# Kernel tuning notes

Hardware: AMD Instinct MI355X
Metric: run time of the kernel (lower is better)

## Reference

```python
import jax, jax.numpy as jnp
from jax import lax
import numpy as np

B, T, F = 256, 2048, 12
EV_VOCAB, RS_VOCAB = 32, 8
EED, RED = 6, 3
H, K = 96, 3
D = F + EED + RED  # 21


def setup_inputs() -> dict:
    key = jax.random.key(0)
    ks = jax.random.split(key, 12)
    s = 0.05
    return {
        'seq': jax.random.normal(ks[0], (B, T, F), jnp.float32),
        'ev': jax.random.randint(ks[1], (B, T), 0, EV_VOCAB),
        'rs': jax.random.randint(ks[2], (B, T), 0, RS_VOCAB),
        'lengths': jax.random.randint(ks[3], (B,), 1, T + 1),  # valid lengths in [1, T]
        'event_emb': jax.random.normal(ks[4], (EV_VOCAB, EED), jnp.float32) * s,
        'result_emb': jax.random.normal(ks[5], (RS_VOCAB, RED), jnp.float32) * s,
        'W_ih': jax.random.normal(ks[6], (4 * H, D), jnp.float32) * s,
        'W_hh': jax.random.normal(ks[7], (4 * H, H), jnp.float32) * s,
        'b_ih': jnp.zeros((4 * H,), jnp.float32),
        'b_hh': jnp.zeros((4 * H,), jnp.float32),
        'W_mlp': jax.random.normal(ks[8], (H, H * K), jnp.float32) * s,
        'b_mlp': jnp.zeros((H,), jnp.float32),
        'W_fc': jax.random.normal(ks[9], (2, 2 * H), jnp.float32) * s,
        'b_fc': jnp.zeros((2,), jnp.float32),
    }


def reference(seq, ev, rs, lengths, event_emb, result_emb, W_ih, W_hh, b_ih, b_hh,
              W_mlp, b_mlp, W_fc, b_fc):
    # embed + concat -> [B,T,D]
    x = jnp.concatenate([seq, event_emb[ev], result_emb[rs]], axis=-1)
    xs = jnp.swapaxes(x, 0, 1)  # [T,B,D]
    ts = jnp.arange(T)
    b = b_ih + b_hh

    def step(carry, inp):
        h, c = carry
        x_t, t = inp
        gates = x_t @ W_ih.T + h @ W_hh.T + b  # [B,4H]
        i, f, g, o = jnp.split(gates, 4, axis=-1)  # PyTorch gate order i,f,g,o
        i = jax.nn.sigmoid(i); f = jax.nn.sigmoid(f)
        g = jnp.tanh(g); o = jax.nn.sigmoid(o)
        c_new = f * c + i * g
        h_new = o * jnp.tanh(c_new)
        m = (t < lengths)[:, None]  # packed-seq semantics: freeze state past length
        h = jnp.where(m, h_new, h)
        c = jnp.where(m, c_new, c)
        out = jnp.where(m, h_new, jnp.zeros_like(h_new))  # pad_packed zeros
        return (h, c), out

    h0 = jnp.zeros((B, H), x.dtype)
    (h_fin, _), outs = lax.scan(step, (h0, h0), (xs, ts))
    out_padded = jnp.swapaxes(outs, 0, 1)  # [B,T,H]

    # vectorized last-k gather (replaces torch Python loop)
    idx = lengths[:, None] - K + jnp.arange(K)  # [B,K]
    valid = idx >= 0
    gathered = jnp.take_along_axis(out_padded, jnp.clip(idx, 0)[:, :, None], axis=1)
    gathered = jnp.where(valid[:, :, None], gathered, jnp.zeros_like(gathered))
    lastk = gathered.reshape(B, K * H)

    h_lastk = jax.nn.relu(lastk @ W_mlp.T + b_mlp)
    h = jnp.concatenate([h_fin, h_lastk], axis=1)  # [B,2H]
    return h @ W_fc.T + b_fc  # [B,2]
```

## Files before the change

### kernel.cpp

```cpp
#include <hip/hip_runtime.h>

#define TT 2048
#define FF 12
#define HH 96
#define NG 384
#define CK 64
#define NT 768
#define L2E 1.44269504088896340736f

typedef __attribute__((ext_vector_type(2))) float f2;
typedef __attribute__((ext_vector_type(4))) float f4;

__device__ __forceinline__ float fast_exp2(float x){ return __builtin_amdgcn_exp2f(x); }
__device__ __forceinline__ float fast_rcp(float x){ return __builtin_amdgcn_rcpf(x); }
__device__ __forceinline__ float sigm(float x){
  return fast_rcp(1.f + fast_exp2(-L2E * x));
}
__device__ __forceinline__ float tanh_f(float x){
  const float e = fast_exp2((-2.f*L2E)*fabsf(x));
  return copysignf((1.f - e) * fast_rcp(1.f + e), x);
}

__global__ __launch_bounds__(NT, 3) void lstm_persist(
  const float* __restrict__ seq, const int* __restrict__ ev, const int* __restrict__ rsi,
  const int* __restrict__ len, const float* __restrict__ eemb, const float* __restrict__ remb,
  const float* __restrict__ W_ih, const float* __restrict__ W_hh,
  const float* __restrict__ b_ih, const float* __restrict__ b_hh,
  const float* __restrict__ W_mlp, const float* __restrict__ b_mlp,
  const float* __restrict__ W_fc, const float* __restrict__ b_fc,
  float* __restrict__ out)
{
  const int b   = blockIdx.x;
  const int tid = threadIdx.x;
  const int w   = tid >> 6;
  const int l   = tid & 63;
  const int s   = w & 3;
  const int gg  = w >> 2;
  const int r0  = 128*gg + l;

  __shared__ __align__(16) float hbuf[2][HH];
  __shared__ __align__(16) float part[NG*5];
  __shared__ __align__(16) float PC[CK*NG];
  __shared__ __align__(16) float xst[CK*24];
  __shared__ __align__(16) float lastk[3*HH];
  __shared__ __align__(16) float tmp[192];
  __shared__ __align__(16) float h2[2*HH];
  __shared__ __align__(16) float et[32*6];
  __shared__ __align__(16) float rt[8*3];
  __shared__ int evb[CK];
  __shared__ int rsb[CK];

  f2 wa[24];
  {
    const float* p0 = W_hh + (size_t)r0*96 + 24*s;
    const float* p1 = W_hh + (size_t)(r0+64)*96 + 24*s;
    #pragma unroll
    for (int j = 0; j < 6; ++j) {
      const f4 q0 = ((const f4*)p0)[j];
      const f4 q1 = ((const f4*)p1)[j];
      wa[2*j]    = q0.xy;  wa[2*j+1]  = q0.zw;
      wa[12+2*j] = q1.xy;  wa[13+2*j] = q1.zw;
    }
  }
  const int th2 = (tid >= NG) ? 1 : 0;
  const int gB  = tid - th2*NG;
  f2 wi2[12];
  {
    float wi[24];
    #pragma unroll
    for (int k = 0; k < 21; ++k) wi[k] = W_ih[gB*21 + k];
    wi[21] = wi[22] = wi[23] = 0.f;
    #pragma unroll
    for (int j = 0; j < 12; ++j) wi2[j] = (f2){wi[2*j], wi[2*j+1]};
  }
  const float bgB = b_ih[gB] + b_hh[gB];

  for (int i = tid; i < 2*HH; i += NT) ((float*)hbuf)[i] = 0.f;
  for (int i = tid; i < 3*HH; i += NT) lastk[i] = 0.f;
  for (int i = tid; i < 192;  i += NT) et[i] = eemb[i];
  for (int i = tid; i < 24;   i += NT) rt[i] = remb[i];

  float c_state = 0.f;
  const int L  = len[b];
  const int ht = tid;

  for (int t = 0; t < L; ++t) {
    const int cr = t & (CK-1);
    if (cr == 0) {
      {
        const int r = tid / 12, c = tid - r*12;
        xst[r*24 + c] = seq[(size_t)b*(TT*FF) + (size_t)t*FF + tid];
        if (tid < CK) {
          evb[tid] = ev [b*TT + t + tid];
          rsb[tid] = rsi[b*TT + t + tid];
        }
      }
      __syncthreads();
      {
        const int r = tid / 12, c2 = tid - r*12 + 12;
        float val;
        if (c2 < 18)      val = et[evb[r]*6 + (c2-12)];
        else if (c2 < 21) val = rt[rsb[r]*3 + (c2-18)];
        else              val = 0.f;
        xst[r*24 + c2] = val;
      }
      __syncthreads();
      {
        #pragma unroll 4
        for (int jj = 0; jj < CK/2; ++jj) {
          const int tr = 2*jj + th2;
          const f4* xp = (const f4*)(xst + tr*24);
          f2 a = (f2){0.f, 0.f};
          #pragma unroll
          for (int j2 = 0; j2 < 6; ++j2) {
            const f4 q = xp[j2];
            a = wi2[2*j2]   * q.xy + a;
            a = wi2[2*j2+1] * q.zw + a;
          }
          PC[tr*NG + gB] = bgB + a.x + a.y;
        }
      }
      __syncthreads();
    }

    {
      const f4* hq = (const f4*)(hbuf[t & 1] + 24*s);
      const f4 q0=hq[0], q1=hq[1], q2=hq[2], q3=hq[3], q4=hq[4], q5=hq[5];
      f2 aA=(f2){0,0}, aB=(f2){0,0}, aC=(f2){0,0}, aD=(f2){0,0};
      aA = wa[0] *q0.xy + aA;  aB = wa[1] *q0.zw + aB;
      aC = wa[12]*q0.xy + aC;  aD = wa[13]*q0.zw + aD;
      aA = wa[2] *q1.xy + aA;  aB = wa[3] *q1.zw + aB;
      aC = wa[14]*q1.xy + aC;  aD = wa[15]*q1.zw + aD;
      aA = wa[4] *q2.xy + aA;  aB = wa[5] *q2.zw + aB;
      aC = wa[16]*q2.xy + aC;  aD = wa[17]*q2.zw + aD;
      aA = wa[6] *q3.xy + aA;  aB = wa[7] *q3.zw + aB;
      aC = wa[18]*q3.xy + aC;  aD = wa[19]*q3.zw + aD;
      aA = wa[8] *q4.xy + aA;  aB = wa[9] *q4.zw + aB;
      aC = wa[20]*q4.xy + aC;  aD = wa[21]*q4.zw + aD;
      aA = wa[10]*q5.xy + aA;  aB = wa[11]*q5.zw + aB;
      aC = wa[22]*q5.xy + aC;  aD = wa[23]*q5.zw + aD;
      part[r0*5 + s]      = aA.x + aA.y + aB.x + aB.y;
      part[(r0+64)*5 + s] = aC.x + aC.y + aD.x + aD.y;
    }
    __syncthreads();

    if (tid < HH) {
      float gv[4];
      #pragma unroll
      for (int gt = 0; gt < 4; ++gt) {
        const int rr = gt*96 + ht;
        const float* pp = part + rr*5;
        gv[gt] = (pp[0] + pp[1]) + (pp[2] + pp[3]) + PC[cr*NG + rr];
      }
      const float gi = sigm(gv[0]);
      const float gf = sigm(gv[1]);
      const float gG = tanh_f(gv[2]);
      const float go = sigm(gv[3]);
      c_state = fmaf(gf, c_state, gi*gG);
      const float hn = go * tanh_f(c_state);
      hbuf[(t+1) & 1][ht] = hn;
      const int kk = t + 3 - L;
      if (kk >= 0) lastk[kk*96 + ht] = hn;
    }
    __syncthreads();
  }

  const float* hfin = hbuf[L & 1];
  if (tid < 192) {
    const int hh = tid / 96;
    const int m  = tid - hh*96;
    const float* wp = W_mlp + m*288 + hh*144;
    const float* xp = lastk + hh*144;
    float sacc = 0.f;
    #pragma unroll 8
    for (int i = 0; i < 144; ++i) sacc = fmaf(wp[i], xp[i], sacc);
    tmp[tid] = sacc;
  }
  __syncthreads();
  if (tid < 96) {
    const float hl = tmp[tid] + tmp[96+tid] + b_mlp[tid];
    h2[96 + tid] = fmaxf(hl, 0.f);
    h2[tid] = hfin[tid];
  }
  __syncthreads();
  if (tid < 128) {
    const int o  = tid >> 6;
    const int ll = tid & 63;
    const float* wf = W_fc + o*192 + 3*ll;
    float sv = fmaf(wf[0], h2[3*ll+0], fmaf(wf[1], h2[3*ll+1], wf[2]*h2[3*ll+2]));
    #pragma unroll
    for (int off = 32; off > 0; off >>= 1) sv += __shfl_down(sv, off);
    if (ll == 0) out[b*2 + o] = sv + b_fc[o];
  }
}

extern "C" void kernel_launch(void* const* d_in, const int* in_sizes, int n_in,
                              void* d_out, int out_size, void* d_ws, size_t ws_size,
                              hipStream_t stream) {
  const float* seq   = (const float*)d_in[0];
  const int*   ev    = (const int*)  d_in[1];
  const int*   rsi   = (const int*)  d_in[2];
  const int*   len   = (const int*)  d_in[3];
  const float* eemb  = (const float*)d_in[4];
  const float* remb  = (const float*)d_in[5];
  const float* W_ih  = (const float*)d_in[6];
  const float* W_hh  = (const float*)d_in[7];
  const float* b_ih  = (const float*)d_in[8];
  const float* b_hh  = (const float*)d_in[9];
  const float* W_mlp = (const float*)d_in[10];
  const float* b_mlp = (const float*)d_in[11];
  const float* W_fc  = (const float*)d_in[12];
  const float* b_fc  = (const float*)d_in[13];

  hipLaunchKernelGGL(lstm_persist, dim3(256), dim3(NT), 0, stream,
                     seq, ev, rsi, len, eemb, remb, W_ih, W_hh, b_ih, b_hh,
                     W_mlp, b_mlp, W_fc, b_fc, (float*)d_out);
}
```

Before: 1.498 ms.

## Reduce gate partial sums with DPP quad shuffles, dropping the per-step barrier

Halves the block to 384 threads. Each group of 4 lanes owns one hidden unit and holds all four gate rows of W_hh for its quarter of the hidden vector. Partial dot products are combined with DPP quad shuffles instead of a shared-memory partial buffer, so one __syncthreads and the serial gate phase on 96 threads are removed from each timestep. All four lanes compute the gate nonlinearities redundantly. In exchange each thread holds 96 weight registers, and the input-projection prologue does twice the work per thread.

```diff
diff --git a/kernel.cpp b/kernel.cpp
--- a/kernel.cpp
+++ b/kernel.cpp
@@ -5,7 +5,7 @@
 #define HH 96
 #define NG 384
 #define CK 64
-#define NT 768
+#define NT 384
 #define L2E 1.44269504088896340736f
 
 typedef __attribute__((ext_vector_type(2))) float f2;
@@ -13,15 +13,19 @@
 
 __device__ __forceinline__ float fast_exp2(float x){ return __builtin_amdgcn_exp2f(x); }
 __device__ __forceinline__ float fast_rcp(float x){ return __builtin_amdgcn_rcpf(x); }
-__device__ __forceinline__ float sigm(float x){
-  return fast_rcp(1.f + fast_exp2(-L2E * x));
-}
+__device__ __forceinline__ float sigm(float x){ return fast_rcp(1.f + fast_exp2(-L2E*x)); }
 __device__ __forceinline__ float tanh_f(float x){
   const float e = fast_exp2((-2.f*L2E)*fabsf(x));
-  return copysignf((1.f - e) * fast_rcp(1.f + e), x);
-}
-
-__global__ __launch_bounds__(NT, 3) void lstm_persist(
+  return copysignf((1.f - e)*fast_rcp(1.f + e), x);
+}
+__device__ __forceinline__ float quad_sum(float x){
+  int y1 = __builtin_amdgcn_update_dpp(0, __float_as_int(x), 0xB1, 0xF, 0xF, true);
+  float s = x + __int_as_float(y1);
+  int y2 = __builtin_amdgcn_update_dpp(0, __float_as_int(s), 0x4E, 0xF, 0xF, true);
+  return s + __int_as_float(y2);
+}
+
+__global__ __launch_bounds__(NT, 2) void lstm_persist(
   const float* __restrict__ seq, const int* __restrict__ ev, const int* __restrict__ rsi,
   const int* __restrict__ len, const float* __restrict__ eemb, const float* __restrict__ remb,
   const float* __restrict__ W_ih, const float* __restrict__ W_hh,
@@ -32,14 +36,10 @@
 {
   const int b   = blockIdx.x;
   const int tid = threadIdx.x;
-  const int w   = tid >> 6;
-  const int l   = tid & 63;
-  const int s   = w & 3;
-  const int gg  = w >> 2;
-  const int r0  = 128*gg + l;
+  const int j   = tid >> 2;
+  const int p   = tid & 3;
 
   __shared__ __align__(16) float hbuf[2][HH];
-  __shared__ __align__(16) float part[NG*5];
   __shared__ __align__(16) float PC[CK*NG];
   __shared__ __align__(16) float xst[CK*24];
   __shared__ __align__(16) float lastk[3*HH];
@@ -50,30 +50,27 @@
   __shared__ int evb[CK];
   __shared__ int rsb[CK];
 
-  f2 wa[24];
-  {
-    const float* p0 = W_hh + (size_t)r0*96 + 24*s;
-    const float* p1 = W_hh + (size_t)(r0+64)*96 + 24*s;
-    #pragma unroll
-    for (int j = 0; j < 6; ++j) {
-      const f4 q0 = ((const f4*)p0)[j];
-      const f4 q1 = ((const f4*)p1)[j];
-      wa[2*j]    = q0.xy;  wa[2*j+1]  = q0.zw;
-      wa[12+2*j] = q1.xy;  wa[13+2*j] = q1.zw;
-    }
-  }
-  const int th2 = (tid >= NG) ? 1 : 0;
-  const int gB  = tid - th2*NG;
+  f2 wr[48];
+  #pragma unroll
+  for (int gt = 0; gt < 4; ++gt) {
+    const float* pw = W_hh + (size_t)(gt*96 + j)*96 + 24*p;
+    #pragma unroll
+    for (int q6 = 0; q6 < 6; ++q6) {
+      const f4 qq = ((const f4*)pw)[q6];
+      wr[gt*12 + 2*q6]     = qq.xy;
+      wr[gt*12 + 2*q6 + 1] = qq.zw;
+    }
+  }
   f2 wi2[12];
   {
     float wi[24];
     #pragma unroll
-    for (int k = 0; k < 21; ++k) wi[k] = W_ih[gB*21 + k];
+    for (int k = 0; k < 21; ++k) wi[k] = W_ih[tid*21 + k];
     wi[21] = wi[22] = wi[23] = 0.f;
     #pragma unroll
-    for (int j = 0; j < 12; ++j) wi2[j] = (f2){wi[2*j], wi[2*j+1]};
-  }
-  const float bgB = b_ih[gB] + b_hh[gB];
+    for (int q6 = 0; q6 < 12; ++q6) wi2[q6] = (f2){wi[2*q6], wi[2*q6+1]};
+  }
+  const float bgB = b_ih[tid] + b_hh[tid];
 
   for (int i = tid; i < 2*HH; i += NT) ((float*)hbuf)[i] = 0.f;
   for (int i = tid; i < 3*HH; i += NT) lastk[i] = 0.f;
@@ -81,23 +78,22 @@
   for (int i = tid; i < 24;   i += NT) rt[i] = remb[i];
 
   float c_state = 0.f;
-  const int L  = len[b];
-  const int ht = tid;
+  const int L = len[b];
 
   for (int t = 0; t < L; ++t) {
     const int cr = t & (CK-1);
     if (cr == 0) {
-      {
-        const int r = tid / 12, c = tid - r*12;
-        xst[r*24 + c] = seq[(size_t)b*(TT*FF) + (size_t)t*FF + tid];
-        if (tid < CK) {
-          evb[tid] = ev [b*TT + t + tid];
-          rsb[tid] = rsi[b*TT + t + tid];
-        }
+      for (int q = tid; q < CK*FF; q += NT) {
+        const int r = q / 12, c = q - r*12;
+        xst[r*24 + c] = seq[(size_t)b*(TT*FF) + (size_t)t*FF + q];
+      }
+      if (tid < CK) {
+        evb[tid] = ev [b*TT + t + tid];
+        rsb[tid] = rsi[b*TT + t + tid];
       }
       __syncthreads();
-      {
-        const int r = tid / 12, c2 = tid - r*12 + 12;
+      for (int q = tid; q < CK*12; q += NT) {
+        const int r = q / 12, c2 = q - r*12 + 12;
         float val;
         if (c2 < 18)      val = et[evb[r]*6 + (c2-12)];
         else if (c2 < 21) val = rt[rsb[r]*3 + (c2-18)];
@@ -105,62 +101,56 @@
         xst[r*24 + c2] = val;
       }
       __syncthreads();
-      {
-        #pragma unroll 4
-        for (int jj = 0; jj < CK/2; ++jj) {
-          const int tr = 2*jj + th2;
-          const f4* xp = (const f4*)(xst + tr*24);
-          f2 a = (f2){0.f, 0.f};
-          #pragma unroll
-          for (int j2 = 0; j2 < 6; ++j2) {
-            const f4 q = xp[j2];
-            a = wi2[2*j2]   * q.xy + a;
-            a = wi2[2*j2+1] * q.zw + a;
-          }
-          PC[tr*NG + gB] = bgB + a.x + a.y;
+      #pragma unroll 4
+      for (int tr = 0; tr < CK; ++tr) {
+        const f4* xp = (const f4*)(xst + tr*24);
+        f2 a = (f2){0.f, 0.f};
+        #pragma unroll
+        for (int q6 = 0; q6 < 6; ++q6) {
+          const f4 qq = xp[q6];
+          a = wi2[2*q6]   * qq.xy + a;
+          a = wi2[2*q6+1] * qq.zw + a;
         }
+        PC[tr*NG + tid] = bgB + a.x + a.y;
       }
       __syncthreads();
     }
 
-    {
-      const f4* hq = (const f4*)(hbuf[t & 1] + 24*s);
-      const f4 q0=hq[0], q1=hq[1], q2=hq[2], q3=hq[3], q4=hq[4], q5=hq[5];
-      f2 aA=(f2){0,0}, aB=(f2){0,0}, aC=(f2){0,0}, aD=(f2){0,0};
-      aA = wa[0] *q0.xy + aA;  aB = wa[1] *q0.zw + aB;
-      aC = wa[12]*q0.xy + aC;  aD = wa[13]*q0.zw + aD;
-      aA = wa[2] *q1.xy + aA;  aB = wa[3] *q1.zw + aB;
-      aC = wa[14]*q1.xy + aC;  aD = wa[15]*q1.zw + aD;
-      aA = wa[4] *q2.xy + aA;  aB = wa[5] *q2.zw + aB;
-      aC = wa[16]*q2.xy + aC;  aD = wa[17]*q2.zw + aD;
-      aA = wa[6] *q3.xy + aA;  aB = wa[7] *q3.zw + aB;
-      aC = wa[18]*q3.xy + aC;  aD = wa[19]*q3.zw + aD;
-      aA = wa[8] *q4.xy + aA;  aB = wa[9] *q4.zw + aB;
-      aC = wa[20]*q4.xy + aC;  aD = wa[21]*q4.zw + aD;
-      aA = wa[10]*q5.xy + aA;  aB = wa[11]*q5.zw + aB;
-      aC = wa[22]*q5.xy + aC;  aD = wa[23]*q5.zw + aD;
-      part[r0*5 + s]      = aA.x + aA.y + aB.x + aB.y;
-      part[(r0+64)*5 + s] = aC.x + aC.y + aD.x + aD.y;
-    }
-    __syncthreads();
-
-    if (tid < HH) {
-      float gv[4];
-      #pragma unroll
-      for (int gt = 0; gt < 4; ++gt) {
-        const int rr = gt*96 + ht;
-        const float* pp = part + rr*5;
-        gv[gt] = (pp[0] + pp[1]) + (pp[2] + pp[3]) + PC[cr*NG + rr];
-      }
-      const float gi = sigm(gv[0]);
-      const float gf = sigm(gv[1]);
-      const float gG = tanh_f(gv[2]);
-      const float go = sigm(gv[3]);
-      c_state = fmaf(gf, c_state, gi*gG);
-      const float hn = go * tanh_f(c_state);
-      hbuf[(t+1) & 1][ht] = hn;
+    const float* hb = hbuf[t & 1];
+    const f4* hq = (const f4*)(hb + 24*p);
+    f4 hv[6];
+    #pragma unroll
+    for (int q6 = 0; q6 < 6; ++q6) hv[q6] = hq[q6];
+    const float pci = PC[cr*NG +        j];
+    const float pcf = PC[cr*NG +  96  + j];
+    const float pcg = PC[cr*NG + 192  + j];
+    const float pco = PC[cr*NG + 288  + j];
+
+    f2 ai=(f2){0,0}, af=(f2){0,0}, ag=(f2){0,0}, ao=(f2){0,0};
+    #pragma unroll
+    for (int q6 = 0; q6 < 6; ++q6) {
+      const f4 qq = hv[q6];
+      ai = wr[     2*q6]*qq.xy + ai;  ai = wr[     2*q6+1]*qq.zw + ai;
+      af = wr[12 + 2*q6]*qq.xy + af;  af = wr[12 + 2*q6+1]*qq.zw + af;
+      ag = wr[24 + 2*q6]*qq.xy + ag;  ag = wr[24 + 2*q6+1]*qq.zw + ag;
+      ao = wr[36 + 2*q6]*qq.xy + ao;  ao = wr[36 + 2*q6+1]*qq.zw + ao;
+    }
+    const float si = quad_sum(ai.x + ai.y) + pci;
+    const float sf = quad_sum(af.x + af.y) + pcf;
+    const float sg = quad_sum(ag.x + ag.y) + pcg;
+    const float so = quad_sum(ao.x + ao.y) + pco;
+
+    const float gi = sigm(si);
+    const float gf = sigm(sf);
+    const float gG = tanh_f(sg);
+    const float go = sigm(so);
+    c_state = fmaf(gf, c_state, gi*gG);
+    const float hn = go * tanh_f(c_state);
+
+    if (p == 0) {
+      hbuf[(t+1) & 1][j] = hn;
       const int kk = t + 3 - L;
-      if (kk >= 0) lastk[kk*96 + ht] = hn;
+      if (kk >= 0) lastk[kk*96 + j] = hn;
     }
     __syncthreads();
   }
```

Result: faster. 1.460 ms (-2.6%).
